# Kernel tuning notes

Measured on AMD Instinct MI355X. Metric: run time of the kernel, lower is better.

## Reference

```python
import jax, jax.numpy as jnp
import numpy as np

N = 4096      # tokens per modality
DIM = 514     # input feature dim
OUT = 256     # out_dim (per-head width, head=1)
NC = 2        # num_classes
LN_EPS = 1e-5


def setup_inputs() -> dict:
    key = jax.random.key(0)
    ks = jax.random.split(key, 12)
    def nrm(k, shape, s=0.02):
        return jax.random.normal(k, shape, dtype=jnp.float32) * s
    return {
        "t1": jax.random.normal(ks[0], (N, DIM), dtype=jnp.float32),
        "t2": jax.random.normal(ks[1], (N, DIM), dtype=jnp.float32),
        "t1c": jax.random.normal(ks[2], (N, DIM), dtype=jnp.float32),
        "Wqkv1": nrm(ks[3], (DIM, 3 * OUT)), "bqkv1": jnp.zeros((3 * OUT,), jnp.float32),
        "Wqkv2": nrm(ks[4], (DIM, 3 * OUT)), "bqkv2": jnp.zeros((3 * OUT,), jnp.float32),
        "Wqkv3": nrm(ks[5], (DIM, 3 * OUT)), "bqkv3": jnp.zeros((3 * OUT,), jnp.float32),
        "Wo1": nrm(ks[6], (2 * OUT, DIM)), "bo1": jnp.zeros((DIM,), jnp.float32),
        "Wo2": nrm(ks[7], (2 * OUT, DIM)), "bo2": jnp.zeros((DIM,), jnp.float32),
        "Wo3": nrm(ks[8], (2 * OUT, DIM)), "bo3": jnp.zeros((DIM,), jnp.float32),
        "ln_g": jnp.ones((3 * DIM,), jnp.float32),
        "ln_b": jnp.zeros((3 * DIM,), jnp.float32),
        "Wh": nrm(ks[9], (3 * DIM, NC)), "bh": jnp.zeros((NC,), jnp.float32),
    }


def _forward(t1, t2, t1c, Wqkv1, bqkv1, Wqkv2, bqkv2, Wqkv3, bqkv3,
             Wo1, bo1, Wo2, bo2, Wo3, bo3, ln_g, ln_b, Wh, bh):
    # QKV projections (head=1 so no head reshape needed)
    q1, k1, v1 = jnp.split(t1 @ Wqkv1 + bqkv1, 3, axis=-1)   # each [n, OUT]
    q2, k2, v2 = jnp.split(t2 @ Wqkv2 + bqkv2, 3, axis=-1)
    q3, k3, v3 = jnp.split(t1c @ Wqkv3 + bqkv3, 3, axis=-1)

    # Six cross-attention instances batched into one group dim g=6.
    # Order: out12, out13, out21, out23, out31, out32  (q_x attends to k_y/v_y)
    qs = jnp.stack([q2, q3, q1, q3, q1, q2])                  # [6, n, OUT]
    ks_ = jnp.stack([k1, k1, k2, k2, k3, k3])
    vs = jnp.stack([v1, v1, v2, v2, v3, v3])
    # NOTE: original code applies NO 1/sqrt(d) scale
    attn = jax.nn.softmax(jnp.einsum('gid,gjd->gij', qs, ks_), axis=-1)
    outs = jnp.einsum('gij,gjd->gid', attn, vs)               # [6, n, OUT]
    out12, out13, out21, out23, out31, out32 = outs

    # residual add with duplicated keys, then per-modality output proj + residual
    t1r = jnp.concatenate([out21, out31], -1) + jnp.concatenate([k1, k1], -1)
    t2r = jnp.concatenate([out12, out32], -1) + jnp.concatenate([k2, k2], -1)
    t3r = jnp.concatenate([out13, out23], -1) + jnp.concatenate([k3, k3], -1)
    a1 = t1r @ Wo1 + bo1 + t1                                 # [n, DIM]
    a2 = t2r @ Wo2 + bo2 + t2
    a3 = t3r @ Wo3 + bo3 + t1c

    atten = jnp.concatenate([a1, a2, a3], -1)                 # [n, 3*DIM]
    mu = jnp.mean(atten, axis=-1, keepdims=True)
    var = jnp.var(atten, axis=-1, keepdims=True)
    normed = (atten - mu) * jax.lax.rsqrt(var + LN_EPS) * ln_g + ln_b
    out = normed @ Wh + bh                                    # [n, NC]
    feat = atten[None]                                        # [1, n, 3*DIM]
    return out, feat


def reference(t1, t2, t1c, Wqkv1, bqkv1, Wqkv2, bqkv2, Wqkv3, bqkv3,
              Wo1, bo1, Wo2, bo2, Wo3, bo3, ln_g, ln_b, Wh, bh):
    return _forward(t1, t2, t1c, Wqkv1, bqkv1, Wqkv2, bqkv2, Wqkv3, bqkv3,
                    Wo1, bo1, Wo2, bo2, Wo3, bo3, ln_g, ln_b, Wh, bh)
```

## Files before the change

### kernel.cpp

```cpp
#include <hip/hip_runtime.h>
#include <hip/hip_bf16.h>

typedef unsigned short u16;
typedef unsigned int u32;
typedef __attribute__((ext_vector_type(8))) __bf16 bf16x8;
typedef __attribute__((ext_vector_type(16))) float f32x16;

#define N_TOK 4096
#define DIMF  514
#define KPAD  544
#define OUT3  768
#define OUTD  256
#define RDIM  512
#define FDIM  1542
#define SHIFT 16.0f
#define NCHUNK 4
#define KTILES ((N_TOK / NCHUNK) / 32)

__device__ __forceinline__ bf16x8 ld_frag(const u16* p) {
    return __builtin_bit_cast(bf16x8, *reinterpret_cast<const uint4*>(p));
}
__device__ __forceinline__ u16 f2bf(float x) {
    return __builtin_bit_cast(u16, __float2bfloat16(x));
}
__device__ __forceinline__ float bf2f(u16 u) {
    return __bfloat162float(__builtin_bit_cast(__hip_bfloat16, u));
}
__device__ __forceinline__ f32x16 mfma_b(bf16x8 a, bf16x8 b, f32x16 c) {
    return __builtin_amdgcn_mfma_f32_32x32x16_bf16(a, b, c, 0, 0, 0);
}
__device__ __forceinline__ void gl_lds16(const u16* g, u16* l) {
    __builtin_amdgcn_global_load_lds(
        (const __attribute__((address_space(1))) void*)(g),
        (__attribute__((address_space(3))) void*)(l), 16, 0, 0);
}

__global__ void prep_kernel(const float* __restrict__ t1, const float* __restrict__ t2,
                            const float* __restrict__ t1c,
                            const float* __restrict__ W1, const float* __restrict__ W2,
                            const float* __restrict__ W3,
                            const float* __restrict__ Wo1, const float* __restrict__ Wo2,
                            const float* __restrict__ Wo3,
                            u16* __restrict__ tA, u16* __restrict__ WqkvT,
                            u16* __restrict__ WoT)
{
    int idx = blockIdx.x * blockDim.x + threadIdx.x;
    const int TA_N = 3 * N_TOK * KPAD;
    const int WQ_N = 3 * OUT3 * KPAD;
    const int WO_N = 3 * DIMF * RDIM;
    if (idx < TA_N) {
        int m = idx / (N_TOK * KPAD);
        int rem = idx - m * (N_TOK * KPAD);
        int row = rem / KPAD;
        int col = rem - row * KPAD;
        const float* t = (m == 0) ? t1 : (m == 1) ? t2 : t1c;
        tA[idx] = (col < DIMF) ? f2bf(t[row * DIMF + col]) : (u16)0;
    } else if (idx < TA_N + WQ_N) {
        int i = idx - TA_N;
        int m = i / (OUT3 * KPAD);
        int rem = i - m * (OUT3 * KPAD);
        int n = rem / KPAD;
        int c = rem - n * KPAD;
        const float* W = (m == 0) ? W1 : (m == 1) ? W2 : W3;
        WqkvT[i] = (c < DIMF) ? f2bf(W[c * OUT3 + n]) : (u16)0;
    } else if (idx < TA_N + WQ_N + WO_N) {
        int i = idx - TA_N - WQ_N;
        int m = i / (DIMF * RDIM);
        int rem = i - m * (DIMF * RDIM);
        int n = rem / RDIM;
        int c = rem - n * RDIM;
        const float* W = (m == 0) ? Wo1 : (m == 1) ? Wo2 : Wo3;
        WoT[i] = f2bf(W[c * DIMF + n]);
    }
}

__global__ __launch_bounds__(256, 1) void qkv_gemm(
    const u16* __restrict__ tA, const u16* __restrict__ WqkvT,
    const float* __restrict__ b1, const float* __restrict__ b2, const float* __restrict__ b3,
    u16* __restrict__ qbuf, u16* __restrict__ kbuf, u16* __restrict__ vT)
{
    const int mt = blockIdx.x, nt = blockIdx.y, mod = blockIdx.z;
    const u16* A = tA + mod * (N_TOK * KPAD);
    const u16* B = WqkvT + mod * (OUT3 * KPAD);
    const float* bias = (mod == 0) ? b1 : (mod == 1) ? b2 : b3;

    __shared__ alignas(16) u16 Al[128 * 40];
    __shared__ alignas(16) u16 Bl[128 * 40];

    const int tid = threadIdx.x;
    const int lane = tid & 63;
    const int w = tid >> 6;
    const int wm = w & 1, wn = w >> 1;
    const int l31 = lane & 31, h = lane >> 5;

    f32x16 acc[2][2];
#pragma unroll
    for (int i = 0; i < 2; i++)
#pragma unroll
        for (int j = 0; j < 2; j++)
#pragma unroll
            for (int r = 0; r < 16; r++) acc[i][j][r] = 0.f;

    for (int kt = 0; kt < KPAD / 32; kt++) {
#pragma unroll
        for (int it = 0; it < 2; it++) {
            int idx = it * 256 + tid;
            int row = idx >> 2;
            int c8 = (idx & 3) * 8;
            uint4 va = *reinterpret_cast<const uint4*>(&A[(mt * 128 + row) * KPAD + kt * 32 + c8]);
            *reinterpret_cast<uint4*>(&Al[row * 40 + c8]) = va;
            uint4 vb = *reinterpret_cast<const uint4*>(&B[(nt * 128 + row) * KPAD + kt * 32 + c8]);
            *reinterpret_cast<uint4*>(&Bl[row * 40 + c8]) = vb;
        }
        __syncthreads();
#pragma unroll
        for (int kc = 0; kc < 2; kc++) {
            bf16x8 af[2], bfr[2];
#pragma unroll
            for (int mr = 0; mr < 2; mr++)
                af[mr] = ld_frag(&Al[(wm * 64 + mr * 32 + l31) * 40 + kc * 16 + h * 8]);
#pragma unroll
            for (int nr = 0; nr < 2; nr++)
                bfr[nr] = ld_frag(&Bl[(wn * 64 + nr * 32 + l31) * 40 + kc * 16 + h * 8]);
#pragma unroll
            for (int mr = 0; mr < 2; mr++)
#pragma unroll
                for (int nr = 0; nr < 2; nr++)
                    acc[mr][nr] = mfma_b(af[mr], bfr[nr], acc[mr][nr]);
        }
        __syncthreads();
    }

    u16* qb = qbuf + mod * (N_TOK * OUTD);
    u16* kb = kbuf + mod * (N_TOK * OUTD);
    u16* vb = vT + mod * (OUTD * N_TOK);
#pragma unroll
    for (int mr = 0; mr < 2; mr++)
#pragma unroll
        for (int nr = 0; nr < 2; nr++)
#pragma unroll
            for (int r = 0; r < 16; r++) {
                int row = mt * 128 + wm * 64 + mr * 32 + (r & 3) + 8 * (r >> 2) + 4 * h;
                int col = nt * 128 + wn * 64 + nr * 32 + l31;
                u16 bv = f2bf(acc[mr][nr][r] + bias[col]);
                int cs = col >> 8, cc = col & 255;
                if (cs == 0)      qb[row * OUTD + cc] = bv;
                else if (cs == 1) kb[row * OUTD + cc] = bv;
                else              vb[cc * N_TOK + row] = bv;
            }
}

__global__ __launch_bounds__(256, 2) void attn_kernel(
    const u16* __restrict__ qbuf, const u16* __restrict__ kbuf,
    const u16* __restrict__ vT, u16* __restrict__ Opart, float* __restrict__ lpart)
{
    const int qt = blockIdx.x;
    const int g  = blockIdx.y;
    const int c  = blockIdx.z;
    const int kv = g >> 1;
    const int mn = (kv == 0) ? 1 : 0;
    const int mx = (kv == 2) ? 1 : 2;
    const int qm = (g & 1) ? mx : mn;

    const u16* Qg = qbuf + qm * (N_TOK * OUTD);
    const u16* Kg = kbuf + kv * (N_TOK * OUTD);
    const u16* Vg = vT + kv * (OUTD * N_TOK);
    u16* Op = Opart + ((size_t)(c * 6 + g) * N_TOK + qt * 128) * OUTD;
    float* lp = lpart + (c * 6 + g) * N_TOK + qt * 128;

    __shared__ alignas(16) u16 Fbuf[2][32 * 512];

    const int tid = threadIdx.x;
    const int lane = tid & 63;
    const int w = tid >> 6;
    const int l31 = lane & 31, h = lane >> 5;
    const int q0 = qt * 128 + w * 32;

    auto stage = [&](int k0, u16* dst) {
        if (w < 2) {
#pragma unroll
            for (int fi = 0; fi < 8; fi++) {
                int dc = w * 8 + fi;
                gl_lds16(&Kg[(k0 + l31) * OUTD + dc * 16 + h * 8], dst + dc * 512);
            }
        } else {
#pragma unroll
            for (int fi = 0; fi < 8; fi++) {
                int f = (w - 2) * 8 + fi;
                int nb = f >> 1, half = f & 1;
                gl_lds16(&Vg[(nb * 32 + l31) * N_TOK + k0 + half * 16 + h * 8],
                         dst + (16 + f) * 512);
            }
        }
    };

    const int k0base = c * (N_TOK / NCHUNK);

    stage(k0base, Fbuf[0]);

    bf16x8 qf[16];
#pragma unroll
    for (int dc = 0; dc < 16; dc++)
        qf[dc] = ld_frag(&Qg[(q0 + l31) * OUTD + dc * 16 + h * 8]);

    f32x16 Oacc[8];
#pragma unroll
    for (int nb = 0; nb < 8; nb++)
#pragma unroll
        for (int r = 0; r < 16; r++) Oacc[nb][r] = 0.f;
    float lsum = 0.f;

    __syncthreads();

    for (int kt = 0; kt < KTILES; kt++) {
        const int p = kt & 1;
        if (kt + 1 < KTILES) stage(k0base + (kt + 1) * 32, Fbuf[p ^ 1]);
        const u16* FB = Fbuf[p];

        f32x16 S;
#pragma unroll
        for (int r = 0; r < 16; r++) S[r] = 0.f;
#pragma unroll
        for (int dc = 0; dc < 16; dc++) {
            bf16x8 kf = ld_frag(&FB[dc * 512 + lane * 8]);
            S = mfma_b(kf, qf[dc], S);
        }

        float e[16];
#pragma unroll
        for (int r = 0; r < 16; r++) { e[r] = __expf(S[r] - SHIFT); lsum += e[r]; }
        u32 pk[8];
#pragma unroll
        for (int i = 0; i < 8; i++)
            pk[i] = (u32)f2bf(e[2 * i]) | ((u32)f2bf(e[2 * i + 1]) << 16);
        u32 x[8];
#pragma unroll
        for (int i = 0; i < 8; i++)
            x[i] = (u32)__shfl_xor((int)pk[i], 32, 64);
        uint4 b0, b1;
        b0.x = h ? x[2] : pk[0]; b0.y = h ? x[3] : pk[1];
        b0.z = h ? pk[2] : x[0]; b0.w = h ? pk[3] : x[1];
        b1.x = h ? x[6] : pk[4]; b1.y = h ? x[7] : pk[5];
        b1.z = h ? pk[6] : x[4]; b1.w = h ? pk[7] : x[5];
        bf16x8 pb0 = __builtin_bit_cast(bf16x8, b0);
        bf16x8 pb1 = __builtin_bit_cast(bf16x8, b1);

#pragma unroll
        for (int nb = 0; nb < 8; nb++) {
            bf16x8 vf0 = ld_frag(&FB[(16 + 2 * nb) * 512 + lane * 8]);
            bf16x8 vf1 = ld_frag(&FB[(17 + 2 * nb) * 512 + lane * 8]);
            Oacc[nb] = mfma_b(vf0, pb0, Oacc[nb]);
            Oacc[nb] = mfma_b(vf1, pb1, Oacc[nb]);
        }
        __syncthreads();
    }

    lsum += __shfl_xor(lsum, 32, 64);
    if (lane < 32) lp[w * 32 + lane] = lsum;

    float* Tb = reinterpret_cast<float*>(&Fbuf[0][0]) + w * (32 * 33);
#pragma unroll
    for (int nb = 0; nb < 8; nb++) {
#pragma unroll
        for (int r = 0; r < 16; r++)
            Tb[((r & 3) + 8 * (r >> 2) + 4 * h) * 33 + l31] = Oacc[nb][r];
        __builtin_amdgcn_s_waitcnt(0);
#pragma unroll
        for (int qq = 0; qq < 16; qq++) {
            float v = Tb[l31 * 33 + qq * 2 + h];
            Op[(w * 32 + qq * 2 + h) * OUTD + nb * 32 + l31] = f2bf(v);
        }
        __builtin_amdgcn_s_waitcnt(0);
    }
}

__global__ __launch_bounds__(256, 1) void combine_kernel(
    const u16* __restrict__ Opart, const float* __restrict__ lpart,
    const u16* __restrict__ kbuf, u16* __restrict__ rbuf)
{
    const int q = blockIdx.x;
    const int g = blockIdx.y;
    const int d = threadIdx.x;
    const int kv = g >> 1;
    const int mn = (kv == 0) ? 1 : 0;
    const int mx = (kv == 2) ? 1 : 2;
    const int qm = (g & 1) ? mx : mn;
    const int sm = (qm == 0) ? 1 : 0;
    const int slot = (kv == sm) ? 0 : 1;

    float o = 0.f, l = 0.f;
#pragma unroll
    for (int c = 0; c < NCHUNK; c++) {
        o += bf2f(Opart[((size_t)(c * 6 + g) * N_TOK + q) * OUTD + d]);
        l += lpart[(c * 6 + g) * N_TOK + q];
    }
    float res = o / l + bf2f(kbuf[qm * (N_TOK * OUTD) + q * OUTD + d]);
    rbuf[qm * (size_t)(N_TOK * RDIM) + q * RDIM + slot * OUTD + d] = f2bf(res);
}

__global__ __launch_bounds__(256, 1) void proj_gemm(
    const u16* __restrict__ rbuf, const u16* __restrict__ WoT,
    const float* __restrict__ bo1, const float* __restrict__ bo2, const float* __restrict__ bo3,
    const float* __restrict__ t1, const float* __restrict__ t2, const float* __restrict__ t1c,
    float* __restrict__ feat)
{
    const int mt = blockIdx.x, nt = blockIdx.y, mod = blockIdx.z;
    const u16* A = rbuf + mod * (N_TOK * RDIM);
    const u16* B = WoT + mod * (DIMF * RDIM);
    const float* bias = (mod == 0) ? bo1 : (mod == 1) ? bo2 : bo3;
    const float* tres = (mod == 0) ? t1 : (mod == 1) ? t2 : t1c;

    __shared__ alignas(16) u16 Al[128 * 40];
    __shared__ alignas(16) u16 Bl[128 * 40];

    const int tid = threadIdx.x;
    const int lane = tid & 63;
    const int w = tid >> 6;
    const int wm = w & 1, wn = w >> 1;
    const int l31 = lane & 31, h = lane >> 5;

    f32x16 acc[2][2];
#pragma unroll
    for (int i = 0; i < 2; i++)
#pragma unroll
        for (int j = 0; j < 2; j++)
#pragma unroll
            for (int r = 0; r < 16; r++) acc[i][j][r] = 0.f;

    for (int kt = 0; kt < RDIM / 32; kt++) {
#pragma unroll
        for (int it = 0; it < 2; it++) {
            int idx = it * 256 + tid;
            int row = idx >> 2;
            int c8 = (idx & 3) * 8;
            uint4 va = *reinterpret_cast<const uint4*>(&A[(mt * 128 + row) * RDIM + kt * 32 + c8]);
            *reinterpret_cast<uint4*>(&Al[row * 40 + c8]) = va;
            int n = nt * 128 + row;
            uint4 vb;
            if (n < DIMF) vb = *reinterpret_cast<const uint4*>(&B[n * RDIM + kt * 32 + c8]);
            else { vb.x = vb.y = vb.z = vb.w = 0u; }
            *reinterpret_cast<uint4*>(&Bl[row * 40 + c8]) = vb;
        }
        __syncthreads();
#pragma unroll
        for (int kc = 0; kc < 2; kc++) {
            bf16x8 af[2], bfr[2];
#pragma unroll
            for (int mr = 0; mr < 2; mr++)
                af[mr] = ld_frag(&Al[(wm * 64 + mr * 32 + l31) * 40 + kc * 16 + h * 8]);
#pragma unroll
            for (int nr = 0; nr < 2; nr++)
                bfr[nr] = ld_frag(&Bl[(wn * 64 + nr * 32 + l31) * 40 + kc * 16 + h * 8]);
#pragma unroll
            for (int mr = 0; mr < 2; mr++)
#pragma unroll
                for (int nr = 0; nr < 2; nr++)
                    acc[mr][nr] = mfma_b(af[mr], bfr[nr], acc[mr][nr]);
        }
        __syncthreads();
    }

#pragma unroll
    for (int mr = 0; mr < 2; mr++)
#pragma unroll
        for (int nr = 0; nr < 2; nr++)
#pragma unroll
            for (int r = 0; r < 16; r++) {
                int row = mt * 128 + wm * 64 + mr * 32 + (r & 3) + 8 * (r >> 2) + 4 * h;
                int col = nt * 128 + wn * 64 + nr * 32 + l31;
                if (col < DIMF) {
                    float v = acc[mr][nr][r] + bias[col] + tres[row * DIMF + col];
                    feat[row * FDIM + mod * DIMF + col] = v;
                }
            }
}

__global__ __launch_bounds__(256, 1) void ln_head(
    const float* __restrict__ feat, const float* __restrict__ gam,
    const float* __restrict__ bet, const float* __restrict__ Wh,
    const float* __restrict__ bh, float* __restrict__ out)
{
    const int row = blockIdx.x;
    const float* x = feat + row * FDIM;
    const int tid = threadIdx.x;
    float v[7];
    float s = 0.f, ss = 0.f;
#pragma unroll
    for (int i = 0; i < 7; i++) {
        int idx = tid + i * 256;
        float val = (idx < FDIM) ? x[idx] : 0.f;
        v[i] = val; s += val; ss += val * val;
    }
#pragma unroll
    for (int m = 1; m < 64; m <<= 1) { s += __shfl_xor(s, m, 64); ss += __shfl_xor(ss, m, 64); }
    __shared__ float red[8];
    const int w = tid >> 6, lane = tid & 63;
    if (lane == 0) { red[w] = s; red[4 + w] = ss; }
    __syncthreads();
    s = red[0] + red[1] + red[2] + red[3];
    ss = red[4] + red[5] + red[6] + red[7];
    const float mu = s / (float)FDIM;
    const float var = ss / (float)FDIM - mu * mu;
    const float rstd = rsqrtf(var + 1e-5f);
    float a0 = 0.f, a1 = 0.f;
#pragma unroll
    for (int i = 0; i < 7; i++) {
        int idx = tid + i * 256;
        if (idx < FDIM) {
            float nv = (v[i] - mu) * rstd * gam[idx] + bet[idx];
            a0 += nv * Wh[idx * 2];
            a1 += nv * Wh[idx * 2 + 1];
        }
    }
#pragma unroll
    for (int m = 1; m < 64; m <<= 1) { a0 += __shfl_xor(a0, m, 64); a1 += __shfl_xor(a1, m, 64); }
    __shared__ float red2[8];
    if (lane == 0) { red2[w] = a0; red2[4 + w] = a1; }
    __syncthreads();
    if (tid == 0) {
        out[row * 2 + 0] = red2[0] + red2[1] + red2[2] + red2[3] + bh[0];
        out[row * 2 + 1] = red2[4] + red2[5] + red2[6] + red2[7] + bh[1];
    }
}

extern "C" void kernel_launch(void* const* d_in, const int* in_sizes, int n_in,
                              void* d_out, int out_size, void* d_ws, size_t ws_size,
                              hipStream_t stream)
{
    const float* t1    = (const float*)d_in[0];
    const float* t2    = (const float*)d_in[1];
    const float* t1c   = (const float*)d_in[2];
    const float* Wqkv1 = (const float*)d_in[3];
    const float* bqkv1 = (const float*)d_in[4];
    const float* Wqkv2 = (const float*)d_in[5];
    const float* bqkv2 = (const float*)d_in[6];
    const float* Wqkv3 = (const float*)d_in[7];
    const float* bqkv3 = (const float*)d_in[8];
    const float* Wo1   = (const float*)d_in[9];
    const float* bo1   = (const float*)d_in[10];
    const float* Wo2   = (const float*)d_in[11];
    const float* bo2   = (const float*)d_in[12];
    const float* Wo3   = (const float*)d_in[13];
    const float* bo3   = (const float*)d_in[14];
    const float* ln_g  = (const float*)d_in[15];
    const float* ln_b  = (const float*)d_in[16];
    const float* Wh    = (const float*)d_in[17];
    const float* bh    = (const float*)d_in[18];

    char* ws = (char*)d_ws;
    size_t off = 0;
    u16* tA    = (u16*)(ws + off); off += (size_t)3 * N_TOK * KPAD * 2;
    u16* WqkvT = (u16*)(ws + off); off += (size_t)3 * OUT3 * KPAD * 2;
    u16* WoT   = (u16*)(ws + off); off += (size_t)3 * DIMF * RDIM * 2;
    u16* qbuf  = (u16*)(ws + off); off += (size_t)3 * N_TOK * OUTD * 2;
    u16* kbuf  = (u16*)(ws + off); off += (size_t)3 * N_TOK * OUTD * 2;
    u16* vT    = (u16*)(ws + off); off += (size_t)3 * OUTD * N_TOK * 2;
    u16* rbuf  = (u16*)(ws + off); off += (size_t)3 * N_TOK * RDIM * 2;
    u16* Opart = (u16*)(ws + off); off += (size_t)NCHUNK * 6 * N_TOK * OUTD * 2;
    float* lpart = (float*)(ws + off); off += (size_t)NCHUNK * 6 * N_TOK * 4;

    float* out  = (float*)d_out;
    float* feat = out + N_TOK * 2;

    const int prep_total = 3 * N_TOK * KPAD + 3 * OUT3 * KPAD + 3 * DIMF * RDIM;
    prep_kernel<<<(prep_total + 255) / 256, 256, 0, stream>>>(
        t1, t2, t1c, Wqkv1, Wqkv2, Wqkv3, Wo1, Wo2, Wo3, tA, WqkvT, WoT);

    qkv_gemm<<<dim3(32, 6, 3), 256, 0, stream>>>(
        tA, WqkvT, bqkv1, bqkv2, bqkv3, qbuf, kbuf, vT);

    attn_kernel<<<dim3(32, 6, NCHUNK), 256, 0, stream>>>(qbuf, kbuf, vT, Opart, lpart);

    combine_kernel<<<dim3(N_TOK, 6), 256, 0, stream>>>(Opart, lpart, kbuf, rbuf);

    proj_gemm<<<dim3(32, 5, 3), 256, 0, stream>>>(
        rbuf, WoT, bo1, bo2, bo3, t1, t2, t1c, feat);

    ln_head<<<4096, 256, 0, stream>>>(feat, ln_g, ln_b, Wh, bh, out);
}
```

Measured before the change: 335.8 us.

## Split prep into tiled transposes, atomic split-K attention reduction, exp2 softmax

Replaces the monolithic prep kernel with a flat activation cast plus LDS-tiled weight transposes that give coalesced reads and writes. The V output of the QKV GEMM is staged through shared memory so the transposed store is vectorised. Q is pre-scaled by log2(e) so the softmax uses exp2 with an equivalent shift. The attention key range is split into 8 chunks instead of 4, with partial O and l accumulated via float atomics into a zeroed buffer, which simplifies the combine step. The atomics and the extra zeroing pass add contention and memory traffic, and the atomic summation order is nondeterministic.

```diff
diff --git a/kernel.cpp b/kernel.cpp
--- a/kernel.cpp
+++ b/kernel.cpp
@@ -13,8 +13,9 @@
 #define OUTD  256
 #define RDIM  512
 #define FDIM  1542
-#define SHIFT 16.0f
-#define NCHUNK 4
+#define LOG2E 1.4426950408889634f
+#define SHIFT2 23.083120654223415f
+#define NCHUNK 8
 #define KTILES ((N_TOK / NCHUNK) / 32)
 
 __device__ __forceinline__ bf16x8 ld_frag(const u16* p) {
@@ -35,43 +36,57 @@
         (__attribute__((address_space(3))) void*)(l), 16, 0, 0);
 }
 
-__global__ void prep_kernel(const float* __restrict__ t1, const float* __restrict__ t2,
-                            const float* __restrict__ t1c,
-                            const float* __restrict__ W1, const float* __restrict__ W2,
-                            const float* __restrict__ W3,
-                            const float* __restrict__ Wo1, const float* __restrict__ Wo2,
-                            const float* __restrict__ Wo3,
-                            u16* __restrict__ tA, u16* __restrict__ WqkvT,
-                            u16* __restrict__ WoT)
-{
-    int idx = blockIdx.x * blockDim.x + threadIdx.x;
-    const int TA_N = 3 * N_TOK * KPAD;
-    const int WQ_N = 3 * OUT3 * KPAD;
-    const int WO_N = 3 * DIMF * RDIM;
-    if (idx < TA_N) {
-        int m = idx / (N_TOK * KPAD);
-        int rem = idx - m * (N_TOK * KPAD);
-        int row = rem / KPAD;
-        int col = rem - row * KPAD;
-        const float* t = (m == 0) ? t1 : (m == 1) ? t2 : t1c;
-        tA[idx] = (col < DIMF) ? f2bf(t[row * DIMF + col]) : (u16)0;
-    } else if (idx < TA_N + WQ_N) {
-        int i = idx - TA_N;
-        int m = i / (OUT3 * KPAD);
-        int rem = i - m * (OUT3 * KPAD);
-        int n = rem / KPAD;
-        int c = rem - n * KPAD;
-        const float* W = (m == 0) ? W1 : (m == 1) ? W2 : W3;
-        WqkvT[i] = (c < DIMF) ? f2bf(W[c * OUT3 + n]) : (u16)0;
-    } else if (idx < TA_N + WQ_N + WO_N) {
-        int i = idx - TA_N - WQ_N;
-        int m = i / (DIMF * RDIM);
-        int rem = i - m * (DIMF * RDIM);
-        int n = rem / RDIM;
-        int c = rem - n * RDIM;
-        const float* W = (m == 0) ? Wo1 : (m == 1) ? Wo2 : Wo3;
-        WoT[i] = f2bf(W[c * DIMF + n]);
-    }
+__global__ __launch_bounds__(256, 1) void prep_tA(
+    const float* __restrict__ t1, const float* __restrict__ t2,
+    const float* __restrict__ t1c, u16* __restrict__ tA)
+{
+    int idx = blockIdx.x * 256 + threadIdx.x;
+    int m = idx / (N_TOK * KPAD);
+    int rem = idx - m * (N_TOK * KPAD);
+    int row = rem / KPAD;
+    int col = rem - row * KPAD;
+    const float* t = (m == 0) ? t1 : (m == 1) ? t2 : t1c;
+    tA[idx] = (col < DIMF) ? f2bf(t[row * DIMF + col]) : (u16)0;
+}
+
+__global__ __launch_bounds__(256, 1) void transpose_w(
+    const float* __restrict__ Wa, const float* __restrict__ Wb,
+    const float* __restrict__ Wc, u16* __restrict__ Out,
+    int R, int C, int OS)
+{
+    const int bx = blockIdx.x;
+    const int by = blockIdx.y;
+    const int m  = blockIdx.z;
+    const float* W = (m == 0) ? Wa : (m == 1) ? Wb : Wc;
+    u16* O = Out + (size_t)m * C * OS;
+
+    __shared__ u16 Lt[64 * 72];
+    const int tid = threadIdx.x;
+    const int c0 = bx * 64, r0 = by * 64;
+#pragma unroll
+    for (int it = 0; it < 16; it++) {
+        int i = it * 256 + tid;
+        int ri = i >> 6, ci = i & 63;
+        int rr = r0 + ri, cc = c0 + ci;
+        float v = (rr < R && cc < C) ? W[rr * C + cc] : 0.f;
+        Lt[ci * 72 + ri] = f2bf(v);
+    }
+    __syncthreads();
+#pragma unroll
+    for (int it = 0; it < 2; it++) {
+        int i = it * 256 + tid;
+        int ci = i >> 3, seg = i & 7;
+        int n = c0 + ci, col = r0 + seg * 8;
+        if (n < C && col < OS)
+            *reinterpret_cast<uint4*>(&O[(size_t)n * OS + col]) =
+                *reinterpret_cast<const uint4*>(&Lt[ci * 72 + seg * 8]);
+    }
+}
+
+__global__ __launch_bounds__(256, 1) void zero_kernel(float4* __restrict__ p, int n4)
+{
+    int i = blockIdx.x * 256 + threadIdx.x;
+    if (i < n4) { float4 z; z.x = z.y = z.z = z.w = 0.f; p[i] = z; }
 }
 
 __global__ __launch_bounds__(256, 1) void qkv_gemm(
@@ -84,8 +99,9 @@
     const u16* B = WqkvT + mod * (OUT3 * KPAD);
     const float* bias = (mod == 0) ? b1 : (mod == 1) ? b2 : b3;
 
-    __shared__ alignas(16) u16 Al[128 * 40];
-    __shared__ alignas(16) u16 Bl[128 * 40];
+    __shared__ alignas(16) u16 smem[128 * 136];
+    u16* Al = smem;
+    u16* Bl = smem + 128 * 40;
 
     const int tid = threadIdx.x;
     const int lane = tid & 63;
@@ -131,28 +147,51 @@
         __syncthreads();
     }
 
-    u16* qb = qbuf + mod * (N_TOK * OUTD);
-    u16* kb = kbuf + mod * (N_TOK * OUTD);
-    u16* vb = vT + mod * (OUTD * N_TOK);
-#pragma unroll
-    for (int mr = 0; mr < 2; mr++)
-#pragma unroll
-        for (int nr = 0; nr < 2; nr++)
-#pragma unroll
-            for (int r = 0; r < 16; r++) {
-                int row = mt * 128 + wm * 64 + mr * 32 + (r & 3) + 8 * (r >> 2) + 4 * h;
-                int col = nt * 128 + wn * 64 + nr * 32 + l31;
-                u16 bv = f2bf(acc[mr][nr][r] + bias[col]);
-                int cs = col >> 8, cc = col & 255;
-                if (cs == 0)      qb[row * OUTD + cc] = bv;
-                else if (cs == 1) kb[row * OUTD + cc] = bv;
-                else              vb[cc * N_TOK + row] = bv;
-            }
+    if (nt < 4) {
+        u16* qb = qbuf + mod * (N_TOK * OUTD);
+        u16* kb = kbuf + mod * (N_TOK * OUTD);
+#pragma unroll
+        for (int mr = 0; mr < 2; mr++)
+#pragma unroll
+            for (int nr = 0; nr < 2; nr++)
+#pragma unroll
+                for (int r = 0; r < 16; r++) {
+                    int row = mt * 128 + wm * 64 + mr * 32 + (r & 3) + 8 * (r >> 2) + 4 * h;
+                    int col = nt * 128 + wn * 64 + nr * 32 + l31;
+                    float sc = (col < 256) ? LOG2E : 1.0f;
+                    u16 bv = f2bf((acc[mr][nr][r] + bias[col]) * sc);
+                    if (col < 256) qb[row * OUTD + col] = bv;
+                    else           kb[row * OUTD + (col - 256)] = bv;
+                }
+    } else {
+        u16* Tv = smem;
+#pragma unroll
+        for (int mr = 0; mr < 2; mr++)
+#pragma unroll
+            for (int nr = 0; nr < 2; nr++)
+#pragma unroll
+                for (int r = 0; r < 16; r++) {
+                    int row_l = wm * 64 + mr * 32 + (r & 3) + 8 * (r >> 2) + 4 * h;
+                    int d_l = wn * 64 + nr * 32 + l31;
+                    int col_g = nt * 128 + d_l;
+                    Tv[d_l * 136 + row_l] = f2bf(acc[mr][nr][r] + bias[col_g]);
+                }
+        __syncthreads();
+        u16* vb = vT + mod * (OUTD * N_TOK);
+        const int colbase = (nt - 4) * 128;
+#pragma unroll
+        for (int it = 0; it < 8; it++) {
+            int i = it * 256 + tid;
+            int cc = i >> 4, seg = i & 15;
+            *reinterpret_cast<uint4*>(&vb[(colbase + cc) * N_TOK + mt * 128 + seg * 8]) =
+                *reinterpret_cast<const uint4*>(&Tv[cc * 136 + seg * 8]);
+        }
+    }
 }
 
 __global__ __launch_bounds__(256, 2) void attn_kernel(
     const u16* __restrict__ qbuf, const u16* __restrict__ kbuf,
-    const u16* __restrict__ vT, u16* __restrict__ Opart, float* __restrict__ lpart)
+    const u16* __restrict__ vT, float* __restrict__ Og, float* __restrict__ lg)
 {
     const int qt = blockIdx.x;
     const int g  = blockIdx.y;
@@ -165,8 +204,8 @@
     const u16* Qg = qbuf + qm * (N_TOK * OUTD);
     const u16* Kg = kbuf + kv * (N_TOK * OUTD);
     const u16* Vg = vT + kv * (OUTD * N_TOK);
-    u16* Op = Opart + ((size_t)(c * 6 + g) * N_TOK + qt * 128) * OUTD;
-    float* lp = lpart + (c * 6 + g) * N_TOK + qt * 128;
+    float* Op = Og + ((size_t)g * N_TOK + qt * 128) * OUTD;
+    float* lp = lg + g * N_TOK + qt * 128;
 
     __shared__ alignas(16) u16 Fbuf[2][32 * 512];
 
@@ -228,7 +267,7 @@
 
         float e[16];
 #pragma unroll
-        for (int r = 0; r < 16; r++) { e[r] = __expf(S[r] - SHIFT); lsum += e[r]; }
+        for (int r = 0; r < 16; r++) { e[r] = exp2f(S[r] - SHIFT2); lsum += e[r]; }
         u32 pk[8];
 #pragma unroll
         for (int i = 0; i < 8; i++)
@@ -256,7 +295,7 @@
     }
 
     lsum += __shfl_xor(lsum, 32, 64);
-    if (lane < 32) lp[w * 32 + lane] = lsum;
+    if (lane < 32) atomicAdd(&lp[w * 32 + lane], lsum);
 
     float* Tb = reinterpret_cast<float*>(&Fbuf[0][0]) + w * (32 * 33);
 #pragma unroll
@@ -268,14 +307,14 @@
 #pragma unroll
         for (int qq = 0; qq < 16; qq++) {
             float v = Tb[l31 * 33 + qq * 2 + h];
-            Op[(w * 32 + qq * 2 + h) * OUTD + nb * 32 + l31] = f2bf(v);
+            atomicAdd(&Op[(w * 32 + qq * 2 + h) * OUTD + nb * 32 + l31], v);
         }
         __builtin_amdgcn_s_waitcnt(0);
     }
 }
 
 __global__ __launch_bounds__(256, 1) void combine_kernel(
-    const u16* __restrict__ Opart, const float* __restrict__ lpart,
+    const float* __restrict__ Og, const float* __restrict__ lg,
     const u16* __restrict__ kbuf, u16* __restrict__ rbuf)
 {
     const int q = blockIdx.x;
@@ -288,12 +327,8 @@
     const int sm = (qm == 0) ? 1 : 0;
     const int slot = (kv == sm) ? 0 : 1;
 
-    float o = 0.f, l = 0.f;
-#pragma unroll
-    for (int c = 0; c < NCHUNK; c++) {
-        o += bf2f(Opart[((size_t)(c * 6 + g) * N_TOK + q) * OUTD + d]);
-        l += lpart[(c * 6 + g) * N_TOK + q];
-    }
+    float o = Og[((size_t)g * N_TOK + q) * OUTD + d];
+    float l = lg[g * N_TOK + q];
     float res = o / l + bf2f(kbuf[qm * (N_TOK * OUTD) + q * OUTD + d]);
     rbuf[qm * (size_t)(N_TOK * RDIM) + q * RDIM + slot * OUTD + d] = f2bf(res);
 }
@@ -456,22 +491,28 @@
     u16* kbuf  = (u16*)(ws + off); off += (size_t)3 * N_TOK * OUTD * 2;
     u16* vT    = (u16*)(ws + off); off += (size_t)3 * OUTD * N_TOK * 2;
     u16* rbuf  = (u16*)(ws + off); off += (size_t)3 * N_TOK * RDIM * 2;
-    u16* Opart = (u16*)(ws + off); off += (size_t)NCHUNK * 6 * N_TOK * OUTD * 2;
-    float* lpart = (float*)(ws + off); off += (size_t)NCHUNK * 6 * N_TOK * 4;
+    float* Og  = (float*)(ws + off); off += (size_t)6 * N_TOK * OUTD * 4;
+    float* lg  = (float*)(ws + off); off += (size_t)6 * N_TOK * 4;
 
     float* out  = (float*)d_out;
     float* feat = out + N_TOK * 2;
 
-    const int prep_total = 3 * N_TOK * KPAD + 3 * OUT3 * KPAD + 3 * DIMF * RDIM;
-    prep_kernel<<<(prep_total + 255) / 256, 256, 0, stream>>>(
-        t1, t2, t1c, Wqkv1, Wqkv2, Wqkv3, Wo1, Wo2, Wo3, tA, WqkvT, WoT);
+    prep_tA<<<(3 * N_TOK * KPAD) / 256, 256, 0, stream>>>(t1, t2, t1c, tA);
+
+    transpose_w<<<dim3(12, 9, 3), 256, 0, stream>>>(
+        Wqkv1, Wqkv2, Wqkv3, WqkvT, DIMF, OUT3, KPAD);
+    transpose_w<<<dim3(9, 8, 3), 256, 0, stream>>>(
+        Wo1, Wo2, Wo3, WoT, RDIM, DIMF, RDIM);
+
+    const int zero_n4 = (6 * N_TOK * OUTD + 6 * N_TOK) / 4;
+    zero_kernel<<<(zero_n4 + 255) / 256, 256, 0, stream>>>((float4*)Og, zero_n4);
 
     qkv_gemm<<<dim3(32, 6, 3), 256, 0, stream>>>(
         tA, WqkvT, bqkv1, bqkv2, bqkv3, qbuf, kbuf, vT);
 
-    attn_kernel<<<dim3(32, 6, NCHUNK), 256, 0, stream>>>(qbuf, kbuf, vT, Opart, lpart);
-
-    combine_kernel<<<dim3(N_TOK, 6), 256, 0, stream>>>(Opart, lpart, kbuf, rbuf);
+    attn_kernel<<<dim3(32, 6, NCHUNK), 256, 0, stream>>>(qbuf, kbuf, vT, Og, lg);
+
+    combine_kernel<<<dim3(N_TOK, 6), 256, 0, stream>>>(Og, lg, kbuf, rbuf);
 
     proj_gemm<<<dim3(32, 5, 3), 256, 0, stream>>>(
         rbuf, WoT, bo1, bo2, bo3, t1, t2, t1c, feat);
```

Result: slower. 457.7 us (+36.3%).
